# Performance work log

Measured on AMD Instinct MI355X. Metric: run time of the kernel, lower is better.

## Reference

```python
import jax, jax.numpy as jnp
import numpy as np

NEG_SLOPE = 0.2  # PyG GATv2Conv default


def gatv2_layer(h, src, dst, Wl, bl, Wr, br, att, bias, n):
    # h: [N, din]; src/dst: [E'] (self-loops included)
    xl = h @ Wl + bl                      # [N, d] source-side transform (lin_l)
    xr = h @ Wr + br                      # [N, d] target-side transform (lin_r)
    s = xl[src] + xr[dst]                 # [E', d] per-edge gather
    e = jax.nn.leaky_relu(s, NEG_SLOPE) @ att  # [E'] GATv2 score
    # segment softmax over incoming edges of each dst node
    m = jax.ops.segment_max(e, dst, num_segments=n)
    ex = jnp.exp(e - m[dst])
    denom = jax.ops.segment_sum(ex, dst, num_segments=n)
    alpha = ex / denom[dst]               # [E']
    out = jax.ops.segment_sum(alpha[:, None] * xl[src], dst, num_segments=n)
    return out + bias                     # [N, d]


def setup_inputs() -> dict:
    key = jax.random.key(0)
    ks = jax.random.split(key, 9)
    n, e, d, L = 50000, 800000, 64, 3
    x = jax.random.normal(ks[0], (n, d), dtype=jnp.float32)
    edge_index = jax.random.randint(ks[1], (2, e), 0, n, dtype=jnp.int64)
    sc = 1.0 / np.sqrt(d)
    Wl = jax.random.normal(ks[2], (L, d, d), dtype=jnp.float32) * sc
    bl = jnp.zeros((L, d), dtype=jnp.float32)
    Wr = jax.random.normal(ks[3], (L, d, d), dtype=jnp.float32) * sc
    br = jnp.zeros((L, d), dtype=jnp.float32)
    att = jax.random.normal(ks[4], (L, d), dtype=jnp.float32) * sc
    bias = jnp.zeros((L, d), dtype=jnp.float32)
    return {"x": x, "edge_index": edge_index, "Wl": Wl, "bl": bl,
            "Wr": Wr, "br": br, "att": att, "bias": bias}


def reference(x, edge_index, Wl, bl, Wr, br, att, bias):
    n = x.shape[0]
    # PyG GATv2Conv default add_self_loops=True
    loops = jnp.arange(n, dtype=edge_index.dtype)
    src = jnp.concatenate([edge_index[0], loops])
    dst = jnp.concatenate([edge_index[1], loops])
    h = x
    num_layers = Wl.shape[0]
    for i in range(num_layers):
        h_new = jax.nn.relu(
            gatv2_layer(h, src, dst, Wl[i], bl[i], Wr[i], br[i], att[i], bias[i], n))
        # residual: applies at layer 0 too since in_dim == hidden_dim
        h = h_new + h
    return h
```

## Files before the change

### kernel.cpp

```cpp
#include <hip/hip_runtime.h>
#include <hip/hip_bf16.h>
#include <cmath>


#define D 64
#define CB 10
#define NBLK 512


__global__ __launch_bounds__(256) void hist_coarse_kernel(
    const int* __restrict__ ei, int* __restrict__ ghist, int E, int N, int NC) {
  __shared__ int h[64];
  int tid = threadIdx.x, blk = blockIdx.x;
  if (tid < 64) h[tid] = 0;
  __syncthreads();
  for (int eid = blk * 256 + tid; eid < E + N; eid += NBLK * 256) {
    int d = (eid < E) ? ei[E + eid] : (eid - E);
    atomicAdd(&h[d >> CB], 1);
  }
  __syncthreads();
  if (tid < NC) ghist[tid * NBLK + blk] = h[tid];
}

__global__ __launch_bounds__(1024) void scan_coarse_kernel(
    int* __restrict__ g, int* __restrict__ cbase, int* __restrict__ dh,
    int M, int NC, int EP) {
  int tid = threadIdx.x;
  if (tid < 64) dh[tid] = 0;
  int chunk = (M + 1023) / 1024;
  int beg = tid * chunk;
  int end = min(M, beg + chunk);
  int sum = 0;
  for (int i = beg; i < end; ++i) sum += g[i];
  int lane = tid & 63, w = tid >> 6;
  int v = sum;
#pragma unroll
  for (int o = 1; o < 64; o <<= 1) {
    int t = __shfl_up(v, o, 64);
    if (lane >= o) v += t;
  }
  __shared__ int wsum[16], woff[16];
  if (lane == 63) wsum[w] = v;
  __syncthreads();
  if (tid == 0) { int r = 0; for (int i = 0; i < 16; ++i) { woff[i] = r; r += wsum[i]; } }
  __syncthreads();
  int run = woff[w] + (v - sum);
  for (int i = beg; i < end; ++i) {
    int old = g[i];
    g[i] = run;
    if ((i & (NBLK - 1)) == 0) cbase[i / NBLK] = run;
    run += old;
  }
  if (tid == 0) cbase[NC] = EP;
}

__global__ __launch_bounds__(256) void scatter_coarse_kernel(
    const int* __restrict__ ei, const int* __restrict__ g,
    unsigned* __restrict__ rec, int E, int N, int NC) {
  __shared__ int cur[64];
  int tid = threadIdx.x, blk = blockIdx.x;
  if (tid < NC) cur[tid] = g[tid * NBLK + blk];
  __syncthreads();
  for (int eid = blk * 256 + tid; eid < E + N; eid += NBLK * 256) {
    int s, d;
    if (eid < E) { s = ei[eid]; d = ei[E + eid]; }
    else         { s = d = eid - E; }
    int pos = atomicAdd(&cur[d >> CB], 1);
    rec[pos] = ((unsigned)(d & ((1 << CB) - 1)) << 16) | (unsigned)s;
  }
}

__global__ __launch_bounds__(1024) void buildcsr2_kernel(
    const unsigned* __restrict__ rec, const int* __restrict__ cbase,
    int* __restrict__ rowptr, unsigned short* __restrict__ csr_src,
    int* __restrict__ dh, int N, int EP) {
  int c = blockIdx.x, tid = threadIdx.x;
  int bb = cbase[c], be = cbase[c + 1];
  __shared__ int hist[1024], cur[1024];
  __shared__ int dloc[64];
  hist[tid] = 0;
  if (tid < 64) dloc[tid] = 0;
  __syncthreads();
  for (int p = bb + tid; p < be; p += 1024)
    atomicAdd(&hist[rec[p] >> 16], 1);
  __syncthreads();
  int dv = hist[tid];
  int lane = tid & 63, w = tid >> 6;
  int inc = dv;
#pragma unroll
  for (int o = 1; o < 64; o <<= 1) {
    int t = __shfl_up(inc, o, 64);
    if (lane >= o) inc += t;
  }
  __shared__ int wsum[16], woff[16];
  if (lane == 63) wsum[w] = inc;
  __syncthreads();
  if (tid == 0) { int r = 0; for (int i = 0; i < 16; ++i) { woff[i] = r; r += wsum[i]; } }
  __syncthreads();
  int excl = woff[w] + inc - dv;
  cur[tid] = excl;
  int node = (c << CB) + tid;
  if (node < N) {
    rowptr[node] = bb + excl;
    atomicAdd(&dloc[min(dv, 63)], 1);
  }
  if (c == 0 && tid == 0) rowptr[N] = EP;
  __syncthreads();
  if (tid < 64 && dloc[tid]) atomicAdd(&dh[tid], dloc[tid]);
  for (int p = bb + tid; p < be; p += 1024) {
    unsigned r = rec[p];
    int pos = bb + atomicAdd(&cur[r >> 16], 1);
    csr_src[pos] = (unsigned short)(r & 0xFFFFu);
  }
}

__global__ __launch_bounds__(64) void deg_scan_kernel(
    const int* __restrict__ dh, int* __restrict__ dcur) {
  int tid = threadIdx.x;
  int bin = 63 - tid;
  int v = dh[bin];
  int orig = v;
#pragma unroll
  for (int o = 1; o < 64; o <<= 1) {
    int t = __shfl_up(v, o, 64);
    if (tid >= o) v += t;
  }
  dcur[bin] = v - orig;
}

__global__ __launch_bounds__(256) void deg_scatter_kernel(
    const int* __restrict__ rowptr, int* __restrict__ dcur,
    int* __restrict__ perm, int N) {
  __shared__ int cnt[64], base[64], cur2[64];
  int tid = threadIdx.x;
  if (tid < 64) { cnt[tid] = 0; cur2[tid] = 0; }
  __syncthreads();
  int i = blockIdx.x * 256 + tid;
  int bin = 0;
  bool act = (i < N);
  if (act) {
    int deg = rowptr[i + 1] - rowptr[i];
    bin = min(deg, 63);
    atomicAdd(&cnt[bin], 1);
  }
  __syncthreads();
  if (tid < 64 && cnt[tid]) base[tid] = atomicAdd(&dcur[tid], cnt[tid]);
  __syncthreads();
  if (act) {
    int pos = base[bin] + atomicAdd(&cur2[bin], 1);
    perm[pos] = i;
  }
}


__device__ __forceinline__ unsigned short f2bf(float f) {
  unsigned u = __float_as_uint(f);
  return (unsigned short)((u + 0x7FFFu + ((u >> 16) & 1u)) >> 16);
}
__device__ __forceinline__ float bflo(unsigned u) { return __uint_as_float(u << 16); }
__device__ __forceinline__ float bfhi(unsigned u) { return __uint_as_float(u & 0xFFFF0000u); }

__global__ __launch_bounds__(256) void transform_kernel(
    const float* __restrict__ h,
    const float* __restrict__ Wl, const float* __restrict__ bl,
    const float* __restrict__ Wr, const float* __restrict__ br,
    unsigned short* __restrict__ xlh, unsigned short* __restrict__ xrh,
    int N, int ntiles) {
  __shared__ float hs[16][D];
  int tid = threadIdx.x;
  int j = tid & 63;
  float wl[D], wr[D];
#pragma unroll
  for (int k = 0; k < D; ++k) {
    wl[k] = Wl[k * D + j];
    wr[k] = Wr[k * D + j];
  }
  float blj = bl[j], brj = br[j];
  int nl = tid >> 6;
  int lr = tid >> 4, lc = (tid & 15) * 4;
  for (int tile = blockIdx.x; tile < ntiles; tile += gridDim.x) {
    int node0 = tile * 16;
    __syncthreads();
    int n = node0 + lr;
    float4 hv4 = make_float4(0.f, 0.f, 0.f, 0.f);
    if (n < N) hv4 = *reinterpret_cast<const float4*>(&h[(size_t)n * D + lc]);
    *reinterpret_cast<float4*>(&hs[lr][lc]) = hv4;
    __syncthreads();
    for (int g = 0; g < 4; ++g) {
      int local = nl * 4 + g;
      int nn = node0 + local;
      float al = blj, ar = brj;
#pragma unroll
      for (int k4 = 0; k4 < D / 4; ++k4) {
        float4 hv = *reinterpret_cast<const float4*>(&hs[local][k4 * 4]);
        al = fmaf(hv.x, wl[k4 * 4 + 0], al);
        ar = fmaf(hv.x, wr[k4 * 4 + 0], ar);
        al = fmaf(hv.y, wl[k4 * 4 + 1], al);
        ar = fmaf(hv.y, wr[k4 * 4 + 1], ar);
        al = fmaf(hv.z, wl[k4 * 4 + 2], al);
        ar = fmaf(hv.z, wr[k4 * 4 + 2], ar);
        al = fmaf(hv.w, wl[k4 * 4 + 3], al);
        ar = fmaf(hv.w, wr[k4 * 4 + 3], ar);
      }
      if (nn < N) {
        xlh[(size_t)nn * D + j] = f2bf(al);
        xrh[(size_t)nn * D + j] = f2bf(ar);
      }
    }
  }
}


__global__ __launch_bounds__(256, 8) void edge_kernel(
    const unsigned short* __restrict__ xlh, const unsigned short* __restrict__ xrh,
    const float* __restrict__ h_in, const int* __restrict__ rowptr,
    const unsigned short* __restrict__ csr_src, const int* __restrict__ perm,
    const float* __restrict__ att, const float* __restrict__ bias,
    float* __restrict__ h_out, int N) {
  int wv = (blockIdx.x * blockDim.x + threadIdx.x) >> 6;
  int lane = threadIdx.x & 63;
  int g = lane >> 4, l16 = lane & 15;
  int idx = wv * 4 + g;
  if (idx >= N) return;
  int v = perm[idx];
  uint2 xq = *reinterpret_cast<const uint2*>(&xrh[(size_t)v * D + l16 * 4]);
  float4 b4v = *reinterpret_cast<const float4*>(&bias[l16 * 4]);
  float4 hv  = *reinterpret_cast<const float4*>(&h_in[(size_t)v * D + l16 * 4]);
  float4 xr4;
  xr4.x = bflo(xq.x); xr4.y = bfhi(xq.x);
  xr4.z = bflo(xq.y); xr4.w = bfhi(xq.y);
  float4 at4 = *reinterpret_cast<const float4*>(&att[l16 * 4]);
  int beg = rowptr[v], end = rowptr[v + 1];
  int deg = end - beg;
  int glane0 = g << 4;
  float m = -INFINITY, s = 0.f;
  float ax = 0.f, ay = 0.f, az = 0.f, aw = 0.f;
  int us = csr_src[min(beg + l16, end - 1)];
  for (int sc = 0; sc < deg; sc += 16) {
    int us_cur = us;
    if (sc + 16 < deg)
      us = csr_src[min(beg + sc + 16 + l16, end - 1)];
    int nt = min(16, deg - sc);
    for (int cc = 0; cc < nt; cc += 4) {
      float4 xu[4];
      float p[4];
#pragma unroll
      for (int k = 0; k < 4; ++k) {
        int u = __shfl(us_cur, glane0 + cc + k, 64);
        uint2 q = *reinterpret_cast<const uint2*>(&xlh[(size_t)u * D + l16 * 4]);
        xu[k].x = bflo(q.x);
        xu[k].y = bfhi(q.x);
        xu[k].z = bflo(q.y);
        xu[k].w = bfhi(q.y);
        float tx = xu[k].x + xr4.x, ty = xu[k].y + xr4.y;
        float tz = xu[k].z + xr4.z, tw = xu[k].w + xr4.w;
        tx = fmaxf(tx, 0.2f * tx);
        ty = fmaxf(ty, 0.2f * ty);
        tz = fmaxf(tz, 0.2f * tz);
        tw = fmaxf(tw, 0.2f * tw);
        float pp = tx * at4.x;
        pp = fmaf(ty, at4.y, pp);
        pp = fmaf(tz, at4.z, pp);
        pp = fmaf(tw, at4.w, pp);
        pp += __shfl_xor(pp, 1, 64);
        pp += __shfl_xor(pp, 2, 64);
        pp += __shfl_xor(pp, 4, 64);
        pp += __shfl_xor(pp, 8, 64);
        p[k] = (cc + k < nt) ? pp : -INFINITY;
      }
      float pm = fmaxf(fmaxf(p[0], p[1]), fmaxf(p[2], p[3]));
      if (pm > m + 8.0f) {
        float a = __expf(m - pm);
        s *= a; ax *= a; ay *= a; az *= a; aw *= a;
        m = pm;
      }
      float w0 = __expf(p[0] - m);
      float w1 = __expf(p[1] - m);
      float w2 = __expf(p[2] - m);
      float w3 = __expf(p[3] - m);
      s += (w0 + w1) + (w2 + w3);
      ax = fmaf(w0, xu[0].x, fmaf(w1, xu[1].x, fmaf(w2, xu[2].x, fmaf(w3, xu[3].x, ax))));
      ay = fmaf(w0, xu[0].y, fmaf(w1, xu[1].y, fmaf(w2, xu[2].y, fmaf(w3, xu[3].y, ay))));
      az = fmaf(w0, xu[0].z, fmaf(w1, xu[1].z, fmaf(w2, xu[2].z, fmaf(w3, xu[3].z, az))));
      aw = fmaf(w0, xu[0].w, fmaf(w1, xu[1].w, fmaf(w2, xu[2].w, fmaf(w3, xu[3].w, aw))));
    }
  }
  float inv = 1.f / s;
  float4 o;
  o.x = fmaxf(ax * inv + b4v.x, 0.f) + hv.x;
  o.y = fmaxf(ay * inv + b4v.y, 0.f) + hv.y;
  o.z = fmaxf(az * inv + b4v.z, 0.f) + hv.z;
  o.w = fmaxf(aw * inv + b4v.w, 0.f) + hv.w;
  *reinterpret_cast<float4*>(&h_out[(size_t)v * D + l16 * 4]) = o;
}


extern "C" void kernel_launch(void* const* d_in, const int* in_sizes, int n_in,
                              void* d_out, int out_size, void* d_ws, size_t ws_size,
                              hipStream_t stream) {
  const float* x    = (const float*)d_in[0];
  const int*   ei   = (const int*)d_in[1];
  const float* Wl   = (const float*)d_in[2];
  const float* bl   = (const float*)d_in[3];
  const float* Wr   = (const float*)d_in[4];
  const float* br   = (const float*)d_in[5];
  const float* att  = (const float*)d_in[6];
  const float* bias = (const float*)d_in[7];

  int N = in_sizes[0] / D;
  int E = in_sizes[1] / 2;
  int L = in_sizes[2] / (D * D);
  int EP = E + N;
  int NC = (N + (1 << CB) - 1) >> CB;
  int M = NC * NBLK;

  float* hA = (float*)d_ws;
  float* hB = hA + (size_t)N * D;
  unsigned short* xlh = (unsigned short*)(hB + (size_t)N * D);
  unsigned short* xrh = xlh + (size_t)N * D;
  unsigned* rec = (unsigned*)(xrh + (size_t)N * D);
  unsigned short* csr_src = (unsigned short*)(rec + EP);
  int* rowptr   = (int*)(csr_src + ((EP + 1) & ~1));
  int* ghist    = rowptr + (N + 1);
  int* cbase    = ghist + M;
  int* dh       = cbase + (NC + 1);
  int* dcur     = dh + 64;
  int* perm     = dcur + 64;

  hist_coarse_kernel<<<NBLK, 256, 0, stream>>>(ei, ghist, E, N, NC);
  scan_coarse_kernel<<<1, 1024, 0, stream>>>(ghist, cbase, dh, M, NC, EP);
  scatter_coarse_kernel<<<NBLK, 256, 0, stream>>>(ei, ghist, rec, E, N, NC);
  buildcsr2_kernel<<<NC, 1024, 0, stream>>>(rec, cbase, rowptr, csr_src, dh, N, EP);
  deg_scan_kernel<<<1, 64, 0, stream>>>(dh, dcur);
  deg_scatter_kernel<<<(N + 255) / 256, 256, 0, stream>>>(rowptr, dcur, perm, N);

  int ntiles = (N + 15) / 16;
  int nwaves = (N + 3) / 4;
  int nblocks = (nwaves * 64 + 255) / 256;
  const float* h_in = x;
  for (int l = 0; l < L; ++l) {
    float* h_out = (l == L - 1) ? (float*)d_out : ((l % 2 == 0) ? hA : hB);
    transform_kernel<<<512, 256, 0, stream>>>(
        h_in, Wl + (size_t)l * D * D, bl + (size_t)l * D,
        Wr + (size_t)l * D * D, br + (size_t)l * D, xlh, xrh, N, ntiles);
    edge_kernel<<<nblocks, 256, 0, stream>>>(
        xlh, xrh, h_in, rowptr, csr_src, perm, att + (size_t)l * D,
        bias + (size_t)l * D, h_out, N);
    h_in = h_out;
  }
}
```

Baseline: 207.7 us.

## Split each node group into two 8-lane halves gathering 16-byte rows per edge

```diff
diff --git a/kernel.cpp b/kernel.cpp
--- a/kernel.cpp
+++ b/kernel.cpp
@@ -211,7 +211,7 @@
 }
 
 
-__global__ __launch_bounds__(256, 8) void edge_kernel(
+__global__ __launch_bounds__(256, 6) void edge_kernel(
     const unsigned short* __restrict__ xlh, const unsigned short* __restrict__ xrh,
     const float* __restrict__ h_in, const int* __restrict__ rowptr,
     const unsigned short* __restrict__ csr_src, const int* __restrict__ perm,
@@ -219,79 +219,128 @@
     float* __restrict__ h_out, int N) {
   int wv = (blockIdx.x * blockDim.x + threadIdx.x) >> 6;
   int lane = threadIdx.x & 63;
-  int g = lane >> 4, l16 = lane & 15;
+  int g = lane >> 4;
+  int o = (lane >> 3) & 1;
+  int f = lane & 7;
+  int l16 = lane & 15;
   int idx = wv * 4 + g;
   if (idx >= N) return;
   int v = perm[idx];
-  uint2 xq = *reinterpret_cast<const uint2*>(&xrh[(size_t)v * D + l16 * 4]);
-  float4 b4v = *reinterpret_cast<const float4*>(&bias[l16 * 4]);
-  float4 hv  = *reinterpret_cast<const float4*>(&h_in[(size_t)v * D + l16 * 4]);
-  float4 xr4;
-  xr4.x = bflo(xq.x); xr4.y = bfhi(xq.x);
-  xr4.z = bflo(xq.y); xr4.w = bfhi(xq.y);
-  float4 at4 = *reinterpret_cast<const float4*>(&att[l16 * 4]);
+  uint4 xq = *reinterpret_cast<const uint4*>(&xrh[(size_t)v * D + f * 8]);
+  float xr8[8];
+  xr8[0] = bflo(xq.x); xr8[1] = bfhi(xq.x);
+  xr8[2] = bflo(xq.y); xr8[3] = bfhi(xq.y);
+  xr8[4] = bflo(xq.z); xr8[5] = bfhi(xq.z);
+  xr8[6] = bflo(xq.w); xr8[7] = bfhi(xq.w);
+  float4 atA = *reinterpret_cast<const float4*>(&att[f * 8]);
+  float4 atB = *reinterpret_cast<const float4*>(&att[f * 8 + 4]);
+  float4 bA = *reinterpret_cast<const float4*>(&bias[f * 8]);
+  float4 bB = *reinterpret_cast<const float4*>(&bias[f * 8 + 4]);
+  float4 hA = *reinterpret_cast<const float4*>(&h_in[(size_t)v * D + f * 8]);
+  float4 hB = *reinterpret_cast<const float4*>(&h_in[(size_t)v * D + f * 8 + 4]);
   int beg = rowptr[v], end = rowptr[v + 1];
   int deg = end - beg;
   int glane0 = g << 4;
   float m = -INFINITY, s = 0.f;
-  float ax = 0.f, ay = 0.f, az = 0.f, aw = 0.f;
+  float acc[8];
+#pragma unroll
+  for (int i = 0; i < 8; ++i) acc[i] = 0.f;
+  int foff = f << 3;
   int us = csr_src[min(beg + l16, end - 1)];
-  for (int sc = 0; sc < deg; sc += 16) {
+
+#define EDGE_CHUNK(SC, NT)                                                    \
+  {                                                                           \
+    int e0 = (SC) + o, e1 = (SC) + 2 + o;                                     \
+    unsigned u0 = (unsigned)__shfl(us_cur, glane0 + e0, 64);                  \
+    unsigned u1 = (unsigned)__shfl(us_cur, glane0 + e1, 64);                  \
+    uint4 q0 = *reinterpret_cast<const uint4*>(&xlh[(u0 << 6) + foff]);       \
+    uint4 q1 = *reinterpret_cast<const uint4*>(&xlh[(u1 << 6) + foff]);       \
+    float x0[8], x1[8];                                                       \
+    x0[0] = bflo(q0.x); x0[1] = bfhi(q0.x); x0[2] = bflo(q0.y);               \
+    x0[3] = bfhi(q0.y); x0[4] = bflo(q0.z); x0[5] = bfhi(q0.z);               \
+    x0[6] = bflo(q0.w); x0[7] = bfhi(q0.w);                                   \
+    x1[0] = bflo(q1.x); x1[1] = bfhi(q1.x); x1[2] = bflo(q1.y);               \
+    x1[3] = bfhi(q1.y); x1[4] = bflo(q1.z); x1[5] = bfhi(q1.z);               \
+    x1[6] = bflo(q1.w); x1[7] = bfhi(q1.w);                                   \
+    float p0, p1;                                                             \
+    {                                                                         \
+      float t, d0 = 0.f, d1 = 0.f;                                            \
+      t = x0[0] + xr8[0]; t = fmaxf(t, 0.2f * t); d0 = t * atA.x;             \
+      t = x0[1] + xr8[1]; t = fmaxf(t, 0.2f * t); d0 = fmaf(t, atA.y, d0);    \
+      t = x0[2] + xr8[2]; t = fmaxf(t, 0.2f * t); d0 = fmaf(t, atA.z, d0);    \
+      t = x0[3] + xr8[3]; t = fmaxf(t, 0.2f * t); d0 = fmaf(t, atA.w, d0);    \
+      t = x0[4] + xr8[4]; t = fmaxf(t, 0.2f * t); d0 = fmaf(t, atB.x, d0);    \
+      t = x0[5] + xr8[5]; t = fmaxf(t, 0.2f * t); d0 = fmaf(t, atB.y, d0);    \
+      t = x0[6] + xr8[6]; t = fmaxf(t, 0.2f * t); d0 = fmaf(t, atB.z, d0);    \
+      t = x0[7] + xr8[7]; t = fmaxf(t, 0.2f * t); d0 = fmaf(t, atB.w, d0);    \
+      t = x1[0] + xr8[0]; t = fmaxf(t, 0.2f * t); d1 = t * atA.x;             \
+      t = x1[1] + xr8[1]; t = fmaxf(t, 0.2f * t); d1 = fmaf(t, atA.y, d1);    \
+      t = x1[2] + xr8[2]; t = fmaxf(t, 0.2f * t); d1 = fmaf(t, atA.z, d1);    \
+      t = x1[3] + xr8[3]; t = fmaxf(t, 0.2f * t); d1 = fmaf(t, atA.w, d1);    \
+      t = x1[4] + xr8[4]; t = fmaxf(t, 0.2f * t); d1 = fmaf(t, atB.x, d1);    \
+      t = x1[5] + xr8[5]; t = fmaxf(t, 0.2f * t); d1 = fmaf(t, atB.y, d1);    \
+      t = x1[6] + xr8[6]; t = fmaxf(t, 0.2f * t); d1 = fmaf(t, atB.z, d1);    \
+      t = x1[7] + xr8[7]; t = fmaxf(t, 0.2f * t); d1 = fmaf(t, atB.w, d1);    \
+      d0 += __shfl_xor(d0, 1, 64); d1 += __shfl_xor(d1, 1, 64);               \
+      d0 += __shfl_xor(d0, 2, 64); d1 += __shfl_xor(d1, 2, 64);               \
+      d0 += __shfl_xor(d0, 4, 64); d1 += __shfl_xor(d1, 4, 64);               \
+      p0 = (e0 < (NT)) ? d0 : -INFINITY;                                      \
+      p1 = (e1 < (NT)) ? d1 : -INFINITY;                                      \
+    }                                                                         \
+    float pm = fmaxf(p0, p1);                                                 \
+    pm = fmaxf(pm, __shfl_xor(pm, 8, 64));                                    \
+    if (pm > m + 8.0f) {                     \
+      float a = __expf(m - pm);                  \
+      s *= a;                                                                 \
+      _Pragma("unroll")                                                       \
+      for (int i = 0; i < 8; ++i) acc[i] *= a;                                \
+      m = pm;                                                                 \
+    }                                                                         \
+    float w0 = __expf(p0 - m);               \
+    float w1 = __expf(p1 - m);                                                \
+    float sw = w0 + w1;                                                       \
+    sw += __shfl_xor(sw, 8, 64);                                              \
+    s += sw;                                                                  \
+    _Pragma("unroll")                                                         \
+    for (int i = 0; i < 8; ++i)                                               \
+      acc[i] = fmaf(w0, x0[i], fmaf(w1, x1[i], acc[i]));                      \
+  }
+
+  for (int base = 0; base < deg; base += 16) {
     int us_cur = us;
-    if (sc + 16 < deg)
-      us = csr_src[min(beg + sc + 16 + l16, end - 1)];
-    int nt = min(16, deg - sc);
-    for (int cc = 0; cc < nt; cc += 4) {
-      float4 xu[4];
-      float p[4];
-#pragma unroll
-      for (int k = 0; k < 4; ++k) {
-        int u = __shfl(us_cur, glane0 + cc + k, 64);
-        uint2 q = *reinterpret_cast<const uint2*>(&xlh[(size_t)u * D + l16 * 4]);
-        xu[k].x = bflo(q.x);
-        xu[k].y = bfhi(q.x);
-        xu[k].z = bflo(q.y);
-        xu[k].w = bfhi(q.y);
-        float tx = xu[k].x + xr4.x, ty = xu[k].y + xr4.y;
-        float tz = xu[k].z + xr4.z, tw = xu[k].w + xr4.w;
-        tx = fmaxf(tx, 0.2f * tx);
-        ty = fmaxf(ty, 0.2f * ty);
-        tz = fmaxf(tz, 0.2f * tz);
-        tw = fmaxf(tw, 0.2f * tw);
-        float pp = tx * at4.x;
-        pp = fmaf(ty, at4.y, pp);
-        pp = fmaf(tz, at4.z, pp);
-        pp = fmaf(tw, at4.w, pp);
-        pp += __shfl_xor(pp, 1, 64);
-        pp += __shfl_xor(pp, 2, 64);
-        pp += __shfl_xor(pp, 4, 64);
-        pp += __shfl_xor(pp, 8, 64);
-        p[k] = (cc + k < nt) ? pp : -INFINITY;
+    if (base + 16 < deg)
+      us = csr_src[min(beg + base + 16 + l16, end - 1)];
+    int nt = min(16, deg - base);
+    if (nt == 16) {
+      EDGE_CHUNK(0, 16)
+      EDGE_CHUNK(4, 16)
+      EDGE_CHUNK(8, 16)
+      EDGE_CHUNK(12, 16)
+    } else {
+      for (int sc = 0; sc < nt; sc += 4) {
+        EDGE_CHUNK(sc, nt)
       }
-      float pm = fmaxf(fmaxf(p[0], p[1]), fmaxf(p[2], p[3]));
-      if (pm > m + 8.0f) {
-        float a = __expf(m - pm);
-        s *= a; ax *= a; ay *= a; az *= a; aw *= a;
-        m = pm;
-      }
-      float w0 = __expf(p[0] - m);
-      float w1 = __expf(p[1] - m);
-      float w2 = __expf(p[2] - m);
-      float w3 = __expf(p[3] - m);
-      s += (w0 + w1) + (w2 + w3);
-      ax = fmaf(w0, xu[0].x, fmaf(w1, xu[1].x, fmaf(w2, xu[2].x, fmaf(w3, xu[3].x, ax))));
-      ay = fmaf(w0, xu[0].y, fmaf(w1, xu[1].y, fmaf(w2, xu[2].y, fmaf(w3, xu[3].y, ay))));
-      az = fmaf(w0, xu[0].z, fmaf(w1, xu[1].z, fmaf(w2, xu[2].z, fmaf(w3, xu[3].z, az))));
-      aw = fmaf(w0, xu[0].w, fmaf(w1, xu[1].w, fmaf(w2, xu[2].w, fmaf(w3, xu[3].w, aw))));
     }
   }
-  float inv = 1.f / s;
-  float4 o;
-  o.x = fmaxf(ax * inv + b4v.x, 0.f) + hv.x;
-  o.y = fmaxf(ay * inv + b4v.y, 0.f) + hv.y;
-  o.z = fmaxf(az * inv + b4v.z, 0.f) + hv.z;
-  o.w = fmaxf(aw * inv + b4v.w, 0.f) + hv.w;
-  *reinterpret_cast<float4*>(&h_out[(size_t)v * D + l16 * 4]) = o;
+#undef EDGE_CHUNK
+
+#pragma unroll
+  for (int i = 0; i < 8; ++i) acc[i] += __shfl_xor(acc[i], 8, 64);
+  if (o == 0) {
+    float inv = 1.f / s;
+    float4 oA, oB;
+    oA.x = fmaxf(acc[0] * inv + bA.x, 0.f) + hA.x;
+    oA.y = fmaxf(acc[1] * inv + bA.y, 0.f) + hA.y;
+    oA.z = fmaxf(acc[2] * inv + bA.z, 0.f) + hA.z;
+    oA.w = fmaxf(acc[3] * inv + bA.w, 0.f) + hA.w;
+    oB.x = fmaxf(acc[4] * inv + bB.x, 0.f) + hB.x;
+    oB.y = fmaxf(acc[5] * inv + bB.y, 0.f) + hB.y;
+    oB.z = fmaxf(acc[6] * inv + bB.z, 0.f) + hB.z;
+    oB.w = fmaxf(acc[7] * inv + bB.w, 0.f) + hB.w;
+    float* op = &h_out[(size_t)v * D + f * 8];
+    *reinterpret_cast<float4*>(op) = oA;
+    *reinterpret_cast<float4*>(op + 4) = oB;
+  }
 }
 
 
```

New measurement: 208.6 us. Within noise of the previous version (+0.4%).

## Split each CSR row by source half to improve gather locality

Applied to the files above, without the earlier changes.

```diff
diff --git a/kernel.cpp b/kernel.cpp
--- a/kernel.cpp
+++ b/kernel.cpp
@@ -72,17 +72,22 @@
 
 __global__ __launch_bounds__(1024) void buildcsr2_kernel(
     const unsigned* __restrict__ rec, const int* __restrict__ cbase,
-    int* __restrict__ rowptr, unsigned short* __restrict__ csr_src,
-    int* __restrict__ dh, int N, int EP) {
+    int* __restrict__ rowptr, int* __restrict__ rowsplit,
+    unsigned short* __restrict__ csr_src,
+    int* __restrict__ dh, int N, int EP, int NH) {
   int c = blockIdx.x, tid = threadIdx.x;
   int bb = cbase[c], be = cbase[c + 1];
-  __shared__ int hist[1024], cur[1024];
+  __shared__ int hist[1024], histlo[1024], cur[1024], curhi[1024];
   __shared__ int dloc[64];
   hist[tid] = 0;
+  histlo[tid] = 0;
   if (tid < 64) dloc[tid] = 0;
   __syncthreads();
-  for (int p = bb + tid; p < be; p += 1024)
-    atomicAdd(&hist[rec[p] >> 16], 1);
+  for (int p = bb + tid; p < be; p += 1024) {
+    unsigned r = rec[p];
+    atomicAdd(&hist[r >> 16], 1);
+    if ((int)(r & 0xFFFFu) < NH) atomicAdd(&histlo[r >> 16], 1);
+  }
   __syncthreads();
   int dv = hist[tid];
   int lane = tid & 63, w = tid >> 6;
@@ -99,9 +104,11 @@
   __syncthreads();
   int excl = woff[w] + inc - dv;
   cur[tid] = excl;
+  curhi[tid] = excl + histlo[tid];
   int node = (c << CB) + tid;
   if (node < N) {
     rowptr[node] = bb + excl;
+    rowsplit[node] = bb + excl + histlo[tid];
     atomicAdd(&dloc[min(dv, 63)], 1);
   }
   if (c == 0 && tid == 0) rowptr[N] = EP;
@@ -109,8 +116,10 @@
   if (tid < 64 && dloc[tid]) atomicAdd(&dh[tid], dloc[tid]);
   for (int p = bb + tid; p < be; p += 1024) {
     unsigned r = rec[p];
-    int pos = bb + atomicAdd(&cur[r >> 16], 1);
-    csr_src[pos] = (unsigned short)(r & 0xFFFFu);
+    int rt = r >> 16;
+    int src = (int)(r & 0xFFFFu);
+    int pos = bb + ((src < NH) ? atomicAdd(&cur[rt], 1) : atomicAdd(&curhi[rt], 1));
+    csr_src[pos] = (unsigned short)src;
   }
 }
 
@@ -214,6 +223,7 @@
 __global__ __launch_bounds__(256, 8) void edge_kernel(
     const unsigned short* __restrict__ xlh, const unsigned short* __restrict__ xrh,
     const float* __restrict__ h_in, const int* __restrict__ rowptr,
+    const int* __restrict__ rowsplit,
     const unsigned short* __restrict__ csr_src, const int* __restrict__ perm,
     const float* __restrict__ att, const float* __restrict__ bias,
     float* __restrict__ h_out, int N) {
@@ -231,58 +241,64 @@
   xr4.z = bflo(xq.y); xr4.w = bfhi(xq.y);
   float4 at4 = *reinterpret_cast<const float4*>(&att[l16 * 4]);
   int beg = rowptr[v], end = rowptr[v + 1];
-  int deg = end - beg;
+  int spl = rowsplit[v];
   int glane0 = g << 4;
   float m = -INFINITY, s = 0.f;
   float ax = 0.f, ay = 0.f, az = 0.f, aw = 0.f;
-  int us = csr_src[min(beg + l16, end - 1)];
-  for (int sc = 0; sc < deg; sc += 16) {
-    int us_cur = us;
-    if (sc + 16 < deg)
-      us = csr_src[min(beg + sc + 16 + l16, end - 1)];
-    int nt = min(16, deg - sc);
-    for (int cc = 0; cc < nt; cc += 4) {
-      float4 xu[4];
-      float p[4];
-#pragma unroll
-      for (int k = 0; k < 4; ++k) {
-        int u = __shfl(us_cur, glane0 + cc + k, 64);
-        uint2 q = *reinterpret_cast<const uint2*>(&xlh[(size_t)u * D + l16 * 4]);
-        xu[k].x = bflo(q.x);
-        xu[k].y = bfhi(q.x);
-        xu[k].z = bflo(q.y);
-        xu[k].w = bfhi(q.y);
-        float tx = xu[k].x + xr4.x, ty = xu[k].y + xr4.y;
-        float tz = xu[k].z + xr4.z, tw = xu[k].w + xr4.w;
-        tx = fmaxf(tx, 0.2f * tx);
-        ty = fmaxf(ty, 0.2f * ty);
-        tz = fmaxf(tz, 0.2f * tz);
-        tw = fmaxf(tw, 0.2f * tw);
-        float pp = tx * at4.x;
-        pp = fmaf(ty, at4.y, pp);
-        pp = fmaf(tz, at4.z, pp);
-        pp = fmaf(tw, at4.w, pp);
-        pp += __shfl_xor(pp, 1, 64);
-        pp += __shfl_xor(pp, 2, 64);
-        pp += __shfl_xor(pp, 4, 64);
-        pp += __shfl_xor(pp, 8, 64);
-        p[k] = (cc + k < nt) ? pp : -INFINITY;
+  for (int half = 0; half < 2; ++half) {
+    int hb = half ? spl : beg;
+    int he = half ? end : spl;
+    int hd = he - hb;
+    if (hd <= 0) continue;
+    int us = csr_src[min(hb + l16, he - 1)];
+    for (int sc = 0; sc < hd; sc += 16) {
+      int us_cur = us;
+      if (sc + 16 < hd)
+        us = csr_src[min(hb + sc + 16 + l16, he - 1)];
+      int nt = min(16, hd - sc);
+      for (int cc = 0; cc < nt; cc += 4) {
+        float4 xu[4];
+        float p[4];
+#pragma unroll
+        for (int k = 0; k < 4; ++k) {
+          int u = __shfl(us_cur, glane0 + cc + k, 64);
+          uint2 q = *reinterpret_cast<const uint2*>(&xlh[(size_t)u * D + l16 * 4]);
+          xu[k].x = bflo(q.x);
+          xu[k].y = bfhi(q.x);
+          xu[k].z = bflo(q.y);
+          xu[k].w = bfhi(q.y);
+          float tx = xu[k].x + xr4.x, ty = xu[k].y + xr4.y;
+          float tz = xu[k].z + xr4.z, tw = xu[k].w + xr4.w;
+          tx = fmaxf(tx, 0.2f * tx);
+          ty = fmaxf(ty, 0.2f * ty);
+          tz = fmaxf(tz, 0.2f * tz);
+          tw = fmaxf(tw, 0.2f * tw);
+          float pp = tx * at4.x;
+          pp = fmaf(ty, at4.y, pp);
+          pp = fmaf(tz, at4.z, pp);
+          pp = fmaf(tw, at4.w, pp);
+          pp += __shfl_xor(pp, 1, 64);
+          pp += __shfl_xor(pp, 2, 64);
+          pp += __shfl_xor(pp, 4, 64);
+          pp += __shfl_xor(pp, 8, 64);
+          p[k] = (cc + k < nt) ? pp : -INFINITY;
+        }
+        float pm = fmaxf(fmaxf(p[0], p[1]), fmaxf(p[2], p[3]));
+        if (pm > m + 8.0f) {
+          float a = __expf(m - pm);
+          s *= a; ax *= a; ay *= a; az *= a; aw *= a;
+          m = pm;
+        }
+        float w0 = __expf(p[0] - m);
+        float w1 = __expf(p[1] - m);
+        float w2 = __expf(p[2] - m);
+        float w3 = __expf(p[3] - m);
+        s += (w0 + w1) + (w2 + w3);
+        ax = fmaf(w0, xu[0].x, fmaf(w1, xu[1].x, fmaf(w2, xu[2].x, fmaf(w3, xu[3].x, ax))));
+        ay = fmaf(w0, xu[0].y, fmaf(w1, xu[1].y, fmaf(w2, xu[2].y, fmaf(w3, xu[3].y, ay))));
+        az = fmaf(w0, xu[0].z, fmaf(w1, xu[1].z, fmaf(w2, xu[2].z, fmaf(w3, xu[3].z, az))));
+        aw = fmaf(w0, xu[0].w, fmaf(w1, xu[1].w, fmaf(w2, xu[2].w, fmaf(w3, xu[3].w, aw))));
       }
-      float pm = fmaxf(fmaxf(p[0], p[1]), fmaxf(p[2], p[3]));
-      if (pm > m + 8.0f) {
-        float a = __expf(m - pm);
-        s *= a; ax *= a; ay *= a; az *= a; aw *= a;
-        m = pm;
-      }
-      float w0 = __expf(p[0] - m);
-      float w1 = __expf(p[1] - m);
-      float w2 = __expf(p[2] - m);
-      float w3 = __expf(p[3] - m);
-      s += (w0 + w1) + (w2 + w3);
-      ax = fmaf(w0, xu[0].x, fmaf(w1, xu[1].x, fmaf(w2, xu[2].x, fmaf(w3, xu[3].x, ax))));
-      ay = fmaf(w0, xu[0].y, fmaf(w1, xu[1].y, fmaf(w2, xu[2].y, fmaf(w3, xu[3].y, ay))));
-      az = fmaf(w0, xu[0].z, fmaf(w1, xu[1].z, fmaf(w2, xu[2].z, fmaf(w3, xu[3].z, az))));
-      aw = fmaf(w0, xu[0].w, fmaf(w1, xu[1].w, fmaf(w2, xu[2].w, fmaf(w3, xu[3].w, aw))));
     }
   }
   float inv = 1.f / s;
@@ -313,6 +329,7 @@
   int EP = E + N;
   int NC = (N + (1 << CB) - 1) >> CB;
   int M = NC * NBLK;
+  int NH = (N + 1) / 2;
 
   float* hA = (float*)d_ws;
   float* hB = hA + (size_t)N * D;
@@ -321,7 +338,8 @@
   unsigned* rec = (unsigned*)(xrh + (size_t)N * D);
   unsigned short* csr_src = (unsigned short*)(rec + EP);
   int* rowptr   = (int*)(csr_src + ((EP + 1) & ~1));
-  int* ghist    = rowptr + (N + 1);
+  int* rowsplit = rowptr + (N + 1);
+  int* ghist    = rowsplit + N;
   int* cbase    = ghist + M;
   int* dh       = cbase + (NC + 1);
   int* dcur     = dh + 64;
@@ -330,7 +348,8 @@
   hist_coarse_kernel<<<NBLK, 256, 0, stream>>>(ei, ghist, E, N, NC);
   scan_coarse_kernel<<<1, 1024, 0, stream>>>(ghist, cbase, dh, M, NC, EP);
   scatter_coarse_kernel<<<NBLK, 256, 0, stream>>>(ei, ghist, rec, E, N, NC);
-  buildcsr2_kernel<<<NC, 1024, 0, stream>>>(rec, cbase, rowptr, csr_src, dh, N, EP);
+  buildcsr2_kernel<<<NC, 1024, 0, stream>>>(rec, cbase, rowptr, rowsplit,
+                                            csr_src, dh, N, EP, NH);
   deg_scan_kernel<<<1, 64, 0, stream>>>(dh, dcur);
   deg_scatter_kernel<<<(N + 255) / 256, 256, 0, stream>>>(rowptr, dcur, perm, N);
 
@@ -344,7 +363,7 @@
         h_in, Wl + (size_t)l * D * D, bl + (size_t)l * D,
         Wr + (size_t)l * D * D, br + (size_t)l * D, xlh, xrh, N, ntiles);
     edge_kernel<<<nblocks, 256, 0, stream>>>(
-        xlh, xrh, h_in, rowptr, csr_src, perm, att + (size_t)l * D,
+        xlh, xrh, h_in, rowptr, rowsplit, csr_src, perm, att + (size_t)l * D,
         bias + (size_t)l * D, h_out, N);
     h_in = h_out;
   }
```

After: 237.5 us. 14.3% more time.
